# Kernel tuning notes

Hardware: AMD Instinct MI355X
Metric: run time of the kernel (lower is better)

The kernel has to match this reference:

```python
import jax, jax.numpy as jnp
import numpy as np

N_NODES = 100000


def gcn_conv(h, row, col, deg_inv_sqrt, W, b, n_nodes):
    # h: [N, F_in]; PyG GCNConv: linear first, then normalized scatter-add aggregation
    h = h @ W  # [N, F_out]
    norm = deg_inv_sqrt[row] * deg_inv_sqrt[col]  # [E']
    msg = h[row] * norm[:, None]  # gather + scale, [E', F_out]
    out = jax.ops.segment_sum(msg, col, num_segments=n_nodes)  # scatter-add
    return out + b


def setup_inputs() -> dict:
    key = jax.random.key(0)
    ks = jax.random.split(key, 8)
    x = jax.random.normal(ks[0], (N_NODES, 1), dtype=jnp.float32)
    edge_index = jax.random.randint(ks[1], (2, 3200000), 0, N_NODES, dtype=jnp.int64)
    W1 = jax.random.normal(ks[2], (1, 64), dtype=jnp.float32) * 0.5
    b1 = jax.random.normal(ks[3], (64,), dtype=jnp.float32) * 0.1
    W2 = jax.random.normal(ks[4], (64, 32), dtype=jnp.float32) * 0.125
    b2 = jax.random.normal(ks[5], (32,), dtype=jnp.float32) * 0.1
    W3 = jax.random.normal(ks[6], (32, 1), dtype=jnp.float32) * 0.18
    b3 = jax.random.normal(ks[7], (1,), dtype=jnp.float32) * 0.1
    return {"x": x, "edge_index": edge_index, "W1": W1, "b1": b1,
            "W2": W2, "b2": b2, "W3": W3, "b3": b3}


def reference(x, edge_index, W1, b1, W2, b2, W3, b3):
    n = x.shape[0]
    # add self-loops (PyG GCNConv default)
    loops = jnp.arange(n, dtype=edge_index.dtype)
    row = jnp.concatenate([edge_index[0], loops])  # source
    col = jnp.concatenate([edge_index[1], loops])  # target
    # symmetric normalization: deg computed on target nodes with unit edge weight
    deg = jax.ops.segment_sum(jnp.ones_like(col, dtype=x.dtype), col, num_segments=n)
    deg_inv_sqrt = jnp.where(deg > 0, jax.lax.rsqrt(deg), 0.0)

    h = jax.nn.relu(gcn_conv(x, row, col, deg_inv_sqrt, W1, b1, n))
    h = jax.nn.relu(gcn_conv(h, row, col, deg_inv_sqrt, W2, b2, n))
    h = gcn_conv(h, row, col, deg_inv_sqrt, W3, b3, n)  # [N, 1]
    return jax.nn.sigmoid(jnp.sum(h, axis=0))  # [1]
```

## Files before the change

### kernel.cpp

```cpp
#include <hip/hip_runtime.h>
#include <math.h>


#define TB 256
#define TBC 1024
#define TBS 512
#define NPB 128
#define NBMAX 1024
#define CHUNK 8192
#define NCHMAX 512
#define CAPB 6144
#define NBF 1024
#define P8SCALE 64.0f
#define P8INV (1.0f / 64.0f)

__device__ inline int block_scan_incl(int v, int t, int nthreads, int* wsums) {
#pragma unroll
    for (int d = 1; d < 64; d <<= 1) {
        int n = __shfl_up(v, d);
        if ((t & 63) >= d) v += n;
    }
    int wid = t >> 6;
    if ((t & 63) == 63) wsums[wid] = v;
    __syncthreads();
    if (wid == 0) {
        int nw = nthreads >> 6;
        int s = (t < nw) ? wsums[t] : 0;
#pragma unroll
        for (int d = 1; d < 16; d <<= 1) {
            int n = __shfl_up(s, d);
            if (t >= d) s += n;
        }
        if (t < nw) wsums[t] = s;
    }
    __syncthreads();
    if (wid > 0) v += wsums[wid - 1];
    return v;
}

__global__ void k_init(const int* __restrict__ ei, int* __restrict__ flag,
                       int* __restrict__ tot, int NB, float* __restrict__ accum) {
    __shared__ int any_nonzero;
    int t = threadIdx.x;
    if (t == 0) any_nonzero = 0;
    __syncthreads();
    if (t < 128) {
        if (ei[2 * t + 1] != 0) atomicOr(&any_nonzero, 1);
    }
    __syncthreads();
    if (t == 0) { flag[0] = (any_nonzero == 0) ? 1 : 0; accum[0] = 0.f; }
    for (int i = t; i < NB; i += blockDim.x) tot[i] = 0;
}

__global__ __launch_bounds__(TBC) void k_chunksort(
        const int* __restrict__ ei, int E, const int* __restrict__ flag,
        unsigned* __restrict__ sbin, unsigned short* __restrict__ s16,
        int* __restrict__ tot, int NB, int nstride) {
    __shared__ int hist[NBMAX];
    __shared__ int cur[NBMAX];
    __shared__ unsigned stage[CHUNK];
    __shared__ int wsums[TBC / 64];
    int t = threadIdx.x;
    int sh = flag[0];
    int c0 = blockIdx.x * CHUNK;
    int c1 = min(c0 + CHUNK, E);
    int n = c1 - c0;
    for (int i = t; i < NB; i += TBC) hist[i] = 0;
    __syncthreads();
    for (int e = c0 + t; e < c1; e += TBC) {
        int c = ei[(size_t)(E + e) << sh];
        atomicAdd(&hist[c >> 7], 1);
    }
    __syncthreads();
    int v = (t < NB) ? hist[t] : 0;
    int incl = block_scan_incl(v, t, TBC, wsums);
    int excl = incl - v;
    cur[t] = excl;
    if (t < NB) {
        s16[(size_t)blockIdx.x * nstride + t] = (unsigned short)excl;
        if (v) atomicAdd(&tot[t], v);
    }
    if (t == 0) s16[(size_t)blockIdx.x * nstride + NB] = (unsigned short)n;
    __syncthreads();
    for (int e = c0 + t; e < c1; e += TBC) {
        int r = ei[(size_t)e << sh];
        int c = ei[(size_t)(E + e) << sh];
        int rank = atomicAdd(&cur[c >> 7], 1);
        stage[rank] = ((unsigned)(c & 127) << 17) | (unsigned)r;
    }
    __syncthreads();
    unsigned* dst = sbin + (size_t)blockIdx.x * CHUNK;
    for (int i = t; i < n; i += TBC) dst[i] = stage[i];
}

__global__ void k_scanbins(const int* __restrict__ tot, int* __restrict__ binoff,
                           int NB, int E) {
    __shared__ int wsums[1024 / 64];
    int t = threadIdx.x;
    int v = (t < NB) ? tot[t] : 0;
    int incl = block_scan_incl(v, t, 1024, wsums);
    if (t < NB) binoff[t] = incl - v;
    if (t == 0) binoff[NB] = E;
}

__global__ __launch_bounds__(TBS) void k_binsort(
        const unsigned* __restrict__ sbin, const unsigned short* __restrict__ s16,
        const int* __restrict__ binoff, int* __restrict__ srow,
        int* __restrict__ off, int* __restrict__ deg,
        const float* __restrict__ x, float* __restrict__ dis,
        float* __restrict__ y, int N, int nchunk, int nstride) {
    __shared__ unsigned stage[CAPB];
    __shared__ int hist[NPB];
    __shared__ int wsums[TBS / 64];
    int b = blockIdx.x, t = threadIdx.x;
    int b0 = b << 7;
    int nn = min(NPB, N - b0);
    int s0v = 0, v = 0;
    if (t < nchunk) {
        s0v = (int)s16[(size_t)t * nstride + b];
        v = (int)s16[(size_t)t * nstride + b + 1] - s0v;
    }
    int incl = block_scan_incl(v, t, TBS, wsums);
    int myexcl = incl - v;
    if (t < nchunk && v > 0 && myexcl < CAPB) {
        int vc = min(v, CAPB - myexcl);
        const unsigned* src = sbin + (size_t)t * CHUNK + s0v;
        for (int i = 0; i < vc; ++i) stage[myexcl + i] = src[i];
    }
    int bo = binoff[b];
    int cntE = min(binoff[b + 1] - bo, CAPB);
    if (t < NPB) hist[t] = 0;
    __syncthreads();
    for (int i = t; i < cntE; i += TBS) atomicAdd(&hist[stage[i] >> 17], 1);
    __syncthreads();
    int hv = (t < NPB) ? hist[t] : 0;
    int hincl = block_scan_incl(hv, t, TBS, wsums);
    int nexcl = hincl - hv;
    if (t < nn) {
        int node = b0 + t;
        off[node] = bo + nexcl;
        deg[node] = hv;
        float dd = rsqrtf((float)(hv + 1));
        dis[node] = dd;
        y[node] = x[node] * dd;
    }
    __syncthreads();
    if (t < NPB) hist[t] = nexcl;
    __syncthreads();
    for (int i = t; i < cntE; i += TBS) {
        unsigned pk = stage[i];
        int rank = atomicAdd(&hist[pk >> 17], 1);
        srow[bo + rank] = (int)(pk & 0x1FFFF);
    }
}

__global__ __launch_bounds__(TB) void k_layer1(
        const int* __restrict__ off, const int* __restrict__ deg,
        const int* __restrict__ srow, const float* __restrict__ y,
        const float* __restrict__ dis,
        const float* __restrict__ W1, const float* __restrict__ b1,
        const float* __restrict__ W2, unsigned* __restrict__ p8, int N) {
    __shared__ float sW1[64], sb1[64];
    __shared__ float4 sW2[512];
    for (int k = threadIdx.x; k < 64; k += TB) { sW1[k] = W1[k]; sb1[k] = b1[k]; }
    const float4* W2v = (const float4*)W2;
    for (int k = threadIdx.x; k < 512; k += TB) sW2[k] = W2v[k];
    __syncthreads();

    int c = blockIdx.x * TB + threadIdx.x;
    if (c >= N) return;
    int k0 = off[c], nd = deg[c];
    float ss[8];
#pragma unroll
    for (int j = 0; j < 8; ++j) ss[j] = 0.f;
    int k = 0;
    for (; k + 8 <= nd; k += 8) {
        int rr[8];
#pragma unroll
        for (int j = 0; j < 8; ++j) rr[j] = srow[k0 + k + j];
#pragma unroll
        for (int j = 0; j < 8; ++j) ss[j] += y[rr[j]];
    }
    for (; k < nd; ++k) ss[0] += y[srow[k0 + k]];
    float d = dis[c];
    float s_ = (((ss[0] + ss[1]) + (ss[2] + ss[3])) +
                ((ss[4] + ss[5]) + (ss[6] + ss[7])) + y[c]) * d;

    float4 g[8];
#pragma unroll
    for (int jj = 0; jj < 8; ++jj) g[jj] = make_float4(0.f, 0.f, 0.f, 0.f);
    for (int f = 0; f < 64; ++f) {
        float hf = fmaxf(fmaf(s_, sW1[f], sb1[f]), 0.f);
#pragma unroll
        for (int jj = 0; jj < 8; ++jj) {
            float4 w = sW2[f * 8 + jj];
            g[jj].x = fmaf(hf, w.x, g[jj].x);
            g[jj].y = fmaf(hf, w.y, g[jj].y);
            g[jj].z = fmaf(hf, w.z, g[jj].z);
            g[jj].w = fmaf(hf, w.w, g[jj].w);
        }
    }
    float sc = d * P8SCALE;
    unsigned pk[8];
#pragma unroll
    for (int jj = 0; jj < 8; ++jj) {
        unsigned u = 0;
        u = __builtin_amdgcn_cvt_pk_fp8_f32(g[jj].x * sc, g[jj].y * sc, u, false);
        u = __builtin_amdgcn_cvt_pk_fp8_f32(g[jj].z * sc, g[jj].w * sc, u, true);
        pk[jj] = u;
    }
    uint4* pv = (uint4*)&p8[(size_t)c * 8];
    pv[0] = make_uint4(pk[0], pk[1], pk[2], pk[3]);
    pv[1] = make_uint4(pk[4], pk[5], pk[6], pk[7]);
}

__global__ __launch_bounds__(TB) void k_layer2(
        const int* __restrict__ off, const int* __restrict__ deg,
        const int* __restrict__ srow, const unsigned* __restrict__ p8,
        const float* __restrict__ dis, const float* __restrict__ b2,
        const float* __restrict__ W3, float* __restrict__ q, int N) {
    int w = (blockIdx.x * TB + threadIdx.x) >> 6;
    int lane = threadIdx.x & 63;
    int grp = lane >> 3;
    int l8 = lane & 7;
    float a0 = 0.f, a1 = 0.f, a2 = 0.f, a3 = 0.f;
    if (w < N) {
        int k0 = off[w], nd = deg[w];
        for (int base = 0; base < nd; base += 64) {
            int m = min(64, nd - base);
            int idx = 0;
            if (lane < m) idx = srow[k0 + base + lane];
            int rr[8];
            unsigned vv[8];
#pragma unroll
            for (int j = 0; j < 8; ++j) rr[j] = __shfl(idx, grp + 8 * j);
#pragma unroll
            for (int j = 0; j < 8; ++j)
                vv[j] = (grp + 8 * j < m) ? p8[(size_t)rr[j] * 8 + l8] : 0u;
#pragma unroll
            for (int j = 0; j < 8; ++j) {
                auto lo = __builtin_amdgcn_cvt_pk_f32_fp8(vv[j], false);
                auto hi = __builtin_amdgcn_cvt_pk_f32_fp8(vv[j], true);
                a0 += lo[0]; a1 += lo[1]; a2 += hi[0]; a3 += hi[1];
            }
        }
    }
    a0 += __shfl_down(a0, 32); a1 += __shfl_down(a1, 32);
    a2 += __shfl_down(a2, 32); a3 += __shfl_down(a3, 32);
    a0 += __shfl_down(a0, 16); a1 += __shfl_down(a1, 16);
    a2 += __shfl_down(a2, 16); a3 += __shfl_down(a3, 16);
    a0 += __shfl_down(a0, 8);  a1 += __shfl_down(a1, 8);
    a2 += __shfl_down(a2, 8);  a3 += __shfl_down(a3, 8);
    float prod = 0.f;
    float d = (w < N) ? dis[w] : 0.f;
    if (w < N && lane < 8) {
        unsigned v = p8[(size_t)w * 8 + l8];
        auto lo = __builtin_amdgcn_cvt_pk_f32_fp8(v, false);
        auto hi = __builtin_amdgcn_cvt_pk_f32_fp8(v, true);
        float4 b2v = ((const float4*)b2)[l8];
        float4 w3v = ((const float4*)W3)[l8];
        float z0 = fmaf(d, (a0 + lo[0]) * P8INV, b2v.x);
        float z1 = fmaf(d, (a1 + lo[1]) * P8INV, b2v.y);
        float z2 = fmaf(d, (a2 + hi[0]) * P8INV, b2v.z);
        float z3 = fmaf(d, (a3 + hi[1]) * P8INV, b2v.w);
        prod = fmaxf(z0, 0.f) * w3v.x + fmaxf(z1, 0.f) * w3v.y
             + fmaxf(z2, 0.f) * w3v.z + fmaxf(z3, 0.f) * w3v.w;
    }
    prod += __shfl_down(prod, 4);
    prod += __shfl_down(prod, 2);
    prod += __shfl_down(prod, 1);
    if (w < N && lane == 0) q[w] = prod * d;
}

__global__ __launch_bounds__(TB) void k_final(
        const int* __restrict__ off, const int* __restrict__ deg,
        const int* __restrict__ srow, const float* __restrict__ q,
        const float* __restrict__ dis, int N, float* __restrict__ accum) {
    __shared__ float red[TB / 64];
    int wglobal = (blockIdx.x * TB + threadIdx.x) >> 6;
    int nwaves = (gridDim.x * TB) >> 6;
    int lane = threadIdx.x & 63;
    float acc = 0.f;
    for (int w = wglobal; w < N; w += nwaves) {
        int k0 = off[w], nd = deg[w];
        float d = dis[w];
        for (int base = 0; base < nd; base += 64) {
            int k = base + lane;
            if (k < nd) acc = fmaf(d, q[srow[k0 + k]], acc);
        }
        if (lane == 0) acc = fmaf(d, q[w], acc);
    }
    acc += __shfl_down(acc, 32); acc += __shfl_down(acc, 16);
    acc += __shfl_down(acc, 8);  acc += __shfl_down(acc, 4);
    acc += __shfl_down(acc, 2);  acc += __shfl_down(acc, 1);
    if (lane == 0) red[threadIdx.x >> 6] = acc;
    __syncthreads();
    if (threadIdx.x == 0)
        atomicAdd(accum, red[0] + red[1] + red[2] + red[3]);
}

__global__ void k_out(const float* __restrict__ accum, const float* __restrict__ b3,
                      float* __restrict__ out, float Nf) {
    float z = accum[0] + Nf * b3[0];
    out[0] = 1.f / (1.f + expf(-z));
}

extern "C" void kernel_launch(void* const* d_in, const int* in_sizes, int n_in,
                              void* d_out, int out_size, void* d_ws, size_t ws_size,
                              hipStream_t stream) {
    const float* x  = (const float*)d_in[0];
    const int*   ei = (const int*)d_in[1];
    const float* W1 = (const float*)d_in[2];
    const float* b1 = (const float*)d_in[3];
    const float* W2 = (const float*)d_in[4];
    const float* b2 = (const float*)d_in[5];
    const float* W3 = (const float*)d_in[6];
    const float* b3 = (const float*)d_in[7];
    float* out = (float*)d_out;

    const int N = in_sizes[0];
    const int E = in_sizes[1] / 2;
    if (N > (1 << 17)) return;
    const int NB = (N + NPB - 1) >> 7;
    const int nchunk = (E + CHUNK - 1) / CHUNK;
    const int nstride = NB + 1;
    if (NB > NBMAX || nchunk > NCHMAX || nchunk > TBS) return;

    char* w = (char*)d_ws;
    size_t o = 0;
    auto alloc = [&](size_t bytes) -> void* {
        void* ptr = w + o;
        o += (bytes + 255) & ~(size_t)255;
        return ptr;
    };
    int*            flag   = (int*)     alloc(256);
    float*          accum  = (float*)   alloc(256);
    int*            tot    = (int*)     alloc((size_t)NBMAX * 4);
    int*            binoff = (int*)     alloc((size_t)(NBMAX + 1) * 4);
    int*            off    = (int*)     alloc((size_t)N * 4);
    int*            deg    = (int*)     alloc((size_t)N * 4);
    float*          dis    = (float*)   alloc((size_t)N * 4);
    float*          y      = (float*)   alloc((size_t)N * 4);
    float*          q      = (float*)   alloc((size_t)N * 4);
    unsigned*       sbin   = (unsigned*)alloc((size_t)nchunk * CHUNK * 4);
    unsigned short* s16    = (unsigned short*)alloc((size_t)nchunk * nstride * 2);
    int*            srow   = (int*)     alloc(((size_t)E + 64) * 4);
    unsigned*       p8     = (unsigned*)alloc((size_t)N * 32);
    if (o > ws_size) return;

    const int nbN = (N + TB - 1) / TB;
    const int nbWave = (N * 64 + TB - 1) / TB;

    k_init<<<1, 1024, 0, stream>>>(ei, flag, tot, NB, accum);
    k_chunksort<<<nchunk, TBC, 0, stream>>>(ei, E, flag, sbin, s16, tot, NB, nstride);
    k_scanbins<<<1, 1024, 0, stream>>>(tot, binoff, NB, E);
    k_binsort<<<NB, TBS, 0, stream>>>(sbin, s16, binoff, srow, off, deg, x, dis, y, N, nchunk, nstride);
    k_layer1<<<nbN, TB, 0, stream>>>(off, deg, srow, y, dis, W1, b1, W2, p8, N);
    k_layer2<<<nbWave, TB, 0, stream>>>(off, deg, srow, p8, dis, b2, W3, q, N);
    k_final<<<NBF, TB, 0, stream>>>(off, deg, srow, q, dis, N, accum);
    k_out<<<1, 1, 0, stream>>>(accum, b3, out, (float)N);
}
```

Before: 172.6 us.

## Keep packed target index in srow and flatten final reduction per bin

```diff
diff --git a/kernel.cpp b/kernel.cpp
--- a/kernel.cpp
+++ b/kernel.cpp
@@ -10,9 +10,9 @@
 #define CHUNK 8192
 #define NCHMAX 512
 #define CAPB 6144
-#define NBF 1024
 #define P8SCALE 64.0f
 #define P8INV (1.0f / 64.0f)
+#define RMASK 0x1FFFFu
 
 __device__ inline int block_scan_incl(int v, int t, int nthreads, int* wsums) {
 #pragma unroll
@@ -105,7 +105,7 @@
 
 __global__ __launch_bounds__(TBS) void k_binsort(
         const unsigned* __restrict__ sbin, const unsigned short* __restrict__ s16,
-        const int* __restrict__ binoff, int* __restrict__ srow,
+        const int* __restrict__ binoff, unsigned* __restrict__ srow,
         int* __restrict__ off, int* __restrict__ deg,
         const float* __restrict__ x, float* __restrict__ dis,
         float* __restrict__ y, int N, int nchunk, int nstride) {
@@ -150,13 +150,13 @@
     for (int i = t; i < cntE; i += TBS) {
         unsigned pk = stage[i];
         int rank = atomicAdd(&hist[pk >> 17], 1);
-        srow[bo + rank] = (int)(pk & 0x1FFFF);
+        srow[bo + rank] = pk;
     }
 }
 
 __global__ __launch_bounds__(TB) void k_layer1(
         const int* __restrict__ off, const int* __restrict__ deg,
-        const int* __restrict__ srow, const float* __restrict__ y,
+        const unsigned* __restrict__ srow, const float* __restrict__ y,
         const float* __restrict__ dis,
         const float* __restrict__ W1, const float* __restrict__ b1,
         const float* __restrict__ W2, unsigned* __restrict__ p8, int N) {
@@ -175,13 +175,13 @@
     for (int j = 0; j < 8; ++j) ss[j] = 0.f;
     int k = 0;
     for (; k + 8 <= nd; k += 8) {
-        int rr[8];
-#pragma unroll
-        for (int j = 0; j < 8; ++j) rr[j] = srow[k0 + k + j];
+        unsigned rr[8];
+#pragma unroll
+        for (int j = 0; j < 8; ++j) rr[j] = srow[k0 + k + j] & RMASK;
 #pragma unroll
         for (int j = 0; j < 8; ++j) ss[j] += y[rr[j]];
     }
-    for (; k < nd; ++k) ss[0] += y[srow[k0 + k]];
+    for (; k < nd; ++k) ss[0] += y[srow[k0 + k] & RMASK];
     float d = dis[c];
     float s_ = (((ss[0] + ss[1]) + (ss[2] + ss[3])) +
                 ((ss[4] + ss[5]) + (ss[6] + ss[7])) + y[c]) * d;
@@ -216,7 +216,7 @@
 
 __global__ __launch_bounds__(TB) void k_layer2(
         const int* __restrict__ off, const int* __restrict__ deg,
-        const int* __restrict__ srow, const unsigned* __restrict__ p8,
+        const unsigned* __restrict__ srow, const unsigned* __restrict__ p8,
         const float* __restrict__ dis, const float* __restrict__ b2,
         const float* __restrict__ W3, float* __restrict__ q, int N) {
     int w = (blockIdx.x * TB + threadIdx.x) >> 6;
@@ -229,11 +229,12 @@
         for (int base = 0; base < nd; base += 64) {
             int m = min(64, nd - base);
             int idx = 0;
-            if (lane < m) idx = srow[k0 + base + lane];
+            if (lane < m) idx = (int)srow[k0 + base + lane];
             int rr[8];
             unsigned vv[8];
 #pragma unroll
-            for (int j = 0; j < 8; ++j) rr[j] = __shfl(idx, grp + 8 * j);
+            for (int j = 0; j < 8; ++j)
+                rr[j] = __shfl(idx, grp + 8 * j) & RMASK;
 #pragma unroll
             for (int j = 0; j < 8; ++j)
                 vv[j] = (grp + 8 * j < m) ? p8[(size_t)rr[j] * 8 + l8] : 0u;
@@ -273,29 +274,27 @@
 }
 
 __global__ __launch_bounds__(TB) void k_final(
-        const int* __restrict__ off, const int* __restrict__ deg,
-        const int* __restrict__ srow, const float* __restrict__ q,
-        const float* __restrict__ dis, int N, float* __restrict__ accum) {
+        const unsigned* __restrict__ srow, const int* __restrict__ binoff,
+        const float* __restrict__ q, const float* __restrict__ dis,
+        int N, float* __restrict__ accum) {
     __shared__ float red[TB / 64];
-    int wglobal = (blockIdx.x * TB + threadIdx.x) >> 6;
-    int nwaves = (gridDim.x * TB) >> 6;
-    int lane = threadIdx.x & 63;
+    int b = blockIdx.x, t = threadIdx.x;
+    int b0 = b << 7;
+    int s0 = binoff[b], s1 = binoff[b + 1];
     float acc = 0.f;
-    for (int w = wglobal; w < N; w += nwaves) {
-        int k0 = off[w], nd = deg[w];
-        float d = dis[w];
-        for (int base = 0; base < nd; base += 64) {
-            int k = base + lane;
-            if (k < nd) acc = fmaf(d, q[srow[k0 + k]], acc);
-        }
-        if (lane == 0) acc = fmaf(d, q[w], acc);
-    }
+    for (int i = s0 + t; i < s1; i += TB) {
+        unsigned pk = srow[i];
+        acc = fmaf(q[pk & RMASK], dis[b0 + (pk >> 17)], acc);
+    }
+    int node = b0 + t;
+    if (t < NPB && node < N) acc = fmaf(dis[node], q[node], acc);
     acc += __shfl_down(acc, 32); acc += __shfl_down(acc, 16);
     acc += __shfl_down(acc, 8);  acc += __shfl_down(acc, 4);
     acc += __shfl_down(acc, 2);  acc += __shfl_down(acc, 1);
-    if (lane == 0) red[threadIdx.x >> 6] = acc;
-    __syncthreads();
-    if (threadIdx.x == 0)
+    int lane = t & 63;
+    if (lane == 0) red[t >> 6] = acc;
+    __syncthreads();
+    if (t == 0)
         atomicAdd(accum, red[0] + red[1] + red[2] + red[3]);
 }
 
@@ -344,7 +343,7 @@
     float*          q      = (float*)   alloc((size_t)N * 4);
     unsigned*       sbin   = (unsigned*)alloc((size_t)nchunk * CHUNK * 4);
     unsigned short* s16    = (unsigned short*)alloc((size_t)nchunk * nstride * 2);
-    int*            srow   = (int*)     alloc(((size_t)E + 64) * 4);
+    unsigned*       srow   = (unsigned*)alloc(((size_t)E + 64) * 4);
     unsigned*       p8     = (unsigned*)alloc((size_t)N * 32);
     if (o > ws_size) return;
 
@@ -357,6 +356,6 @@
     k_binsort<<<NB, TBS, 0, stream>>>(sbin, s16, binoff, srow, off, deg, x, dis, y, N, nchunk, nstride);
     k_layer1<<<nbN, TB, 0, stream>>>(off, deg, srow, y, dis, W1, b1, W2, p8, N);
     k_layer2<<<nbWave, TB, 0, stream>>>(off, deg, srow, p8, dis, b2, W3, q, N);
-    k_final<<<NBF, TB, 0, stream>>>(off, deg, srow, q, dis, N, accum);
+    k_final<<<NB, TB, 0, stream>>>(srow, binoff, q, dis, N, accum);
     k_out<<<1, 1, 0, stream>>>(accum, b3, out, (float)N);
 }
```

Result: faster. 153.4 us (median of 4 runs) (-11.1%).
